# Kernel tuning notes

Measured on AMD Instinct MI355X. Metric: run time of the kernel, lower is better.

## Reference

```python
import jax, jax.numpy as jnp
import numpy as np

QMAX = 127.0          # int8 symmetric range
MMA_ALPHA = 1024.0    # leap mmaAlpha; applied to one scale and removed from the other (net no-op)
EPS = 1e-12


def _dynamic_quantize(t):
    """Per-tensor (blockSize=-1) symmetric int8 dynamic quantization."""
    s = jnp.maximum(jnp.max(jnp.abs(t)) / QMAX, EPS)
    q = jnp.clip(jnp.round(t / s), -QMAX, QMAX).astype(jnp.int8)
    return q, s


def setup_inputs() -> dict:
    key = jax.random.key(0)
    k1, k2 = jax.random.split(key)
    x = jax.random.normal(k1, (8192, 256), dtype=jnp.float32)   # [M, K]
    y = jax.random.normal(k2, (256, 8192), dtype=jnp.float32)   # [K, N]
    return {"x": x, "y": y}


def reference(x, y):
    x_q, x_s = _dynamic_quantize(x)
    y_q, y_s = _dynamic_quantize(y)
    # Integer accumulation (K=256 * 127^2 fits easily in int32), then dequantize.
    acc = jnp.matmul(x_q.astype(jnp.int32), y_q.astype(jnp.int32))  # [M, N] int32
    # mmaAlpha rescaling: scale one operand's scale up by alpha, the other down; cancels exactly.
    out = acc.astype(jnp.float32) * ((x_s * MMA_ALPHA) * (y_s / MMA_ALPHA))
    return out
```

## Files before the change

### kernel.cpp

```cpp
#include <hip/hip_runtime.h>

#define M_DIM 8192
#define N_DIM 8192
#define K_DIM 256

typedef __attribute__((ext_vector_type(4))) int i32x4;
typedef __attribute__((ext_vector_type(4))) float f32x4;

__device__ __forceinline__ void bar_lds() {
    asm volatile("s_waitcnt lgkmcnt(0)" ::: "memory");
    __builtin_amdgcn_sched_barrier(0);
    __builtin_amdgcn_s_barrier();
}

__device__ __forceinline__ void bar_stage() {
    asm volatile("s_waitcnt vmcnt(0) lgkmcnt(0)" ::: "memory");
    __builtin_amdgcn_sched_barrier(0);
    __builtin_amdgcn_s_barrier();
}

__device__ __forceinline__ void async_lds16(const signed char* g, signed char* l) {
    __builtin_amdgcn_global_load_lds(
        (const __attribute__((address_space(1))) void*)g,
        (__attribute__((address_space(3))) void*)l, 16, 0, 0);
}

__global__ __launch_bounds__(256) void absmax_kernel(const float* __restrict__ x,
                                                     const float* __restrict__ y,
                                                     float* __restrict__ partial) {
    const float* p = (blockIdx.y == 0) ? x : y;
    const int n4 = (M_DIM * K_DIM) / 4;
    const float4* p4 = (const float4*)p;
    float m = 0.0f;
    for (int i = blockIdx.x * 256 + threadIdx.x; i < n4; i += 256 * 256) {
        float4 v = p4[i];
        m = fmaxf(m, fmaxf(fmaxf(fabsf(v.x), fabsf(v.y)), fmaxf(fabsf(v.z), fabsf(v.w))));
    }
    for (int off = 32; off > 0; off >>= 1)
        m = fmaxf(m, __shfl_down(m, off));
    __shared__ float sm[4];
    int wid = threadIdx.x >> 6;
    if ((threadIdx.x & 63) == 0) sm[wid] = m;
    __syncthreads();
    if (threadIdx.x == 0)
        partial[blockIdx.y * 256 + blockIdx.x] = fmaxf(fmaxf(sm[0], sm[1]), fmaxf(sm[2], sm[3]));
}

__device__ __forceinline__ void load_scales(const float* __restrict__ partial,
                                            float& sx, float& sy, float* ssc) {
    const int tid = threadIdx.x;
    float mx = partial[tid];
    float my = partial[256 + tid];
    for (int off = 32; off > 0; off >>= 1) {
        mx = fmaxf(mx, __shfl_down(mx, off));
        my = fmaxf(my, __shfl_down(my, off));
    }
    if ((tid & 63) == 0) { ssc[tid >> 6] = mx; ssc[4 + (tid >> 6)] = my; }
    __syncthreads();
    mx = fmaxf(fmaxf(ssc[0], ssc[1]), fmaxf(ssc[2], ssc[3]));
    my = fmaxf(fmaxf(ssc[4], ssc[5]), fmaxf(ssc[6], ssc[7]));
    sx = fmaxf(mx / 127.0f, 1e-12f);
    sy = fmaxf(my / 127.0f, 1e-12f);
}

__device__ __forceinline__ int quant1(float v, float s) {
    float q = rintf(v / s);
    q = fmaxf(-127.0f, fminf(127.0f, q));
    return (int)q;
}

__global__ __launch_bounds__(256) void quant_kernel(const float* __restrict__ x,
                                                    const float* __restrict__ y,
                                                    unsigned int* __restrict__ xq_w,
                                                    signed char* __restrict__ yqt,
                                                    const float* __restrict__ partial) {
    __shared__ float ssc[8];
    __shared__ signed char tile[64][68];
    float sx, sy;
    load_scales(partial, sx, sy, ssc);
    int b = blockIdx.x;
    const int t = threadIdx.x;
    if (b < 2048) {
        int i = b * 256 + t;
        float4 v = ((const float4*)x)[i];
        unsigned b0 = (unsigned)quant1(v.x, sx) & 0xFF;
        unsigned b1 = (unsigned)quant1(v.y, sx) & 0xFF;
        unsigned b2 = (unsigned)quant1(v.z, sx) & 0xFF;
        unsigned b3 = (unsigned)quant1(v.w, sx) & 0xFF;
        xq_w[i] = b0 | (b1 << 8) | (b2 << 16) | (b3 << 24);
    } else {
        b -= 2048;
        const int n0 = (b & 127) * 64;
        const int k0 = (b >> 7) * 64;
        #pragma unroll
        for (int r = 0; r < 16; ++r) {
            int idx = r * 256 + t;
            int k = idx >> 6, n = idx & 63;
            float v = y[(size_t)(k0 + k) * N_DIM + n0 + n];
            tile[k][n] = (signed char)quant1(v, sy);
        }
        __syncthreads();
        #pragma unroll
        for (int r = 0; r < 4; ++r) {
            int idx = r * 256 + t;
            int n = idx >> 4, kw = idx & 15;
            unsigned w = ((unsigned)(unsigned char)tile[kw * 4 + 0][n])
                       | ((unsigned)(unsigned char)tile[kw * 4 + 1][n] << 8)
                       | ((unsigned)(unsigned char)tile[kw * 4 + 2][n] << 16)
                       | ((unsigned)(unsigned char)tile[kw * 4 + 3][n] << 24);
            *(unsigned*)(yqt + (size_t)(n0 + n) * K_DIM + k0 + kw * 4) = w;
        }
    }
}

__global__ __launch_bounds__(256) void gemm_i8_kernel(const signed char* __restrict__ xq,
                                                      const signed char* __restrict__ yqt,
                                                      const float* __restrict__ partial,
                                                      float* __restrict__ out) {
    __shared__ __align__(16) unsigned char smem[32 * 132 * 4];
    __shared__ float ssc[8];
    signed char* sA = (signed char*)smem;
    signed char* sB = sA + 128 * 64;
    float (*epi)[132] = (float(*)[132])smem;

    float sx, sy;
    load_scales(partial, sx, sy, ssc);
    const float scale = (sx * 1024.0f) * (sy / 1024.0f);

    const int tid = threadIdx.x;
    const int w = tid >> 6;
    const int lane = tid & 63;
    const int wr = w >> 1, wc = w & 1;

    const signed char* gbase = (w < 2)
        ? (xq  + (size_t)(blockIdx.y * 128 + (w & 1) * 64 + (lane >> 2)) * K_DIM + (lane & 3) * 16)
        : (yqt + (size_t)(blockIdx.x * 128 + (w & 1) * 64 + (lane >> 2)) * K_DIM + (lane & 3) * 16);
    signed char* lbase = ((w < 2) ? sA : sB) + (w & 1) * 64 * 64;

    const int frow = lane & 15;
    const int fk = (lane >> 4) * 16;
    const signed char* ard = sA + (wr * 64 + frow) * 64 + fk;
    const signed char* brd = sB + (wc * 64 + frow) * 64 + fk;

    i32x4 acc[4][4] = {};
    #pragma unroll
    for (int ks = 0; ks < 4; ++ks) {
        if (ks) bar_lds();
        #pragma unroll
        for (int c = 0; c < 4; ++c)
            async_lds16(gbase + (size_t)(c * 16) * K_DIM + ks * 64, lbase + c * 16 * 64);
        bar_stage();
        i32x4 a[4], b[4];
        #pragma unroll
        for (int mi = 0; mi < 4; ++mi)
            a[mi] = *(const i32x4*)(ard + mi * 16 * 64);
        #pragma unroll
        for (int ni = 0; ni < 4; ++ni)
            b[ni] = *(const i32x4*)(brd + ni * 16 * 64);
        #pragma unroll
        for (int mi = 0; mi < 4; ++mi)
            #pragma unroll
            for (int ni = 0; ni < 4; ++ni)
                acc[mi][ni] = __builtin_amdgcn_mfma_i32_16x16x64_i8(a[mi], b[ni], acc[mi][ni], 0, 0, 0);
    }
    bar_lds();

    const int qrow = (lane >> 4) * 4;
    const int qcol = lane & 15;
    #pragma unroll
    for (int mi = 0; mi < 4; ++mi) {
        if (mi) bar_lds();
        #pragma unroll
        for (int ni = 0; ni < 4; ++ni)
            #pragma unroll
            for (int r = 0; r < 4; ++r)
                epi[wr * 16 + qrow + r][wc * 64 + ni * 16 + qcol] =
                    (float)acc[mi][ni][r] * scale;
        bar_lds();
        #pragma unroll
        for (int i = 0; i < 4; ++i) {
            int row = i * 8 + (tid >> 5);
            int col4 = tid & 31;
            f32x4 v = *(const f32x4*)&epi[row][col4 * 4];
            int grow = blockIdx.y * 128 + (row >> 4) * 64 + mi * 16 + (row & 15);
            int gcol = blockIdx.x * 128 + col4 * 4;
            __builtin_nontemporal_store(v, (f32x4*)&out[(size_t)grow * N_DIM + gcol]);
        }
    }
}

extern "C" void kernel_launch(void* const* d_in, const int* in_sizes, int n_in,
                              void* d_out, int out_size, void* d_ws, size_t ws_size,
                              hipStream_t stream) {
    const float* x = (const float*)d_in[0];
    const float* y = (const float*)d_in[1];
    float* out = (float*)d_out;

    unsigned char* ws = (unsigned char*)d_ws;
    float* partial = (float*)ws;
    signed char* xq = (signed char*)(ws + 4096);
    signed char* yqt = xq + (size_t)M_DIM * K_DIM;

    absmax_kernel<<<dim3(256, 2), 256, 0, stream>>>(x, y, partial);

    quant_kernel<<<2048 + 512, 256, 0, stream>>>(x, y, (unsigned int*)xq, yqt, partial);

    gemm_i8_kernel<<<dim3(N_DIM / 128, M_DIM / 128), 256, 0, stream>>>(xq, yqt, partial, out);
}
```

Before: 68.63 us.

## Reshape GEMM block tile to 64x256 with each wave owning a 64-column strip

Changes the int8 GEMM block tile from 128x128 (2x2 waves) to 64 rows by 256 columns, with all four waves sharing the same A rows and each taking a 64-column slice of B. Loads and the epilogue staging buffer are rewritten to match, and the grid becomes 32x128. The intent is to make each output row segment wider for more contiguous stores and to change the A/B load balance. LDS use rises and B traffic per block grows, so the total global load volume shifts toward B.

```diff
diff --git a/kernel.cpp b/kernel.cpp
--- a/kernel.cpp
+++ b/kernel.cpp
@@ -117,11 +117,11 @@
                                                       const signed char* __restrict__ yqt,
                                                       const float* __restrict__ partial,
                                                       float* __restrict__ out) {
-    __shared__ __align__(16) unsigned char smem[32 * 132 * 4];
+    __shared__ __align__(16) unsigned char smem[20480];
     __shared__ float ssc[8];
     signed char* sA = (signed char*)smem;
-    signed char* sB = sA + 128 * 64;
-    float (*epi)[132] = (float(*)[132])smem;
+    signed char* sB = (signed char*)smem + 4096;
+    float (*epi)[260] = (float(*)[260])smem;
 
     float sx, sy;
     load_scales(partial, sx, sy, ssc);
@@ -130,26 +130,28 @@
     const int tid = threadIdx.x;
     const int w = tid >> 6;
     const int lane = tid & 63;
-    const int wr = w >> 1, wc = w & 1;
-
-    const signed char* gbase = (w < 2)
-        ? (xq  + (size_t)(blockIdx.y * 128 + (w & 1) * 64 + (lane >> 2)) * K_DIM + (lane & 3) * 16)
-        : (yqt + (size_t)(blockIdx.x * 128 + (w & 1) * 64 + (lane >> 2)) * K_DIM + (lane & 3) * 16);
-    signed char* lbase = ((w < 2) ? sA : sB) + (w & 1) * 64 * 64;
+    const int by = blockIdx.y;
+    const int bx = blockIdx.x;
 
     const int frow = lane & 15;
     const int fk = (lane >> 4) * 16;
-    const signed char* ard = sA + (wr * 64 + frow) * 64 + fk;
-    const signed char* brd = sB + (wc * 64 + frow) * 64 + fk;
+
+    const signed char* ag = xq + (size_t)(by * 64 + (tid >> 2)) * K_DIM + (tid & 3) * 16;
 
     i32x4 acc[4][4] = {};
     #pragma unroll
     for (int ks = 0; ks < 4; ++ks) {
         if (ks) bar_lds();
-        #pragma unroll
-        for (int c = 0; c < 4; ++c)
-            async_lds16(gbase + (size_t)(c * 16) * K_DIM + ks * 64, lbase + c * 16 * 64);
+        async_lds16(ag + ks * 64, sA + tid * 16);
+        #pragma unroll
+        for (int c = 0; c < 4; ++c) {
+            int i = c * 256 + tid;
+            async_lds16(yqt + (size_t)(bx * 256 + (i >> 2)) * K_DIM + (i & 3) * 16 + ks * 64,
+                        sB + i * 16);
+        }
         bar_stage();
+        const signed char* ard = sA + frow * 64 + fk;
+        const signed char* brd = sB + (w * 64 + frow) * 64 + fk;
         i32x4 a[4], b[4];
         #pragma unroll
         for (int mi = 0; mi < 4; ++mi)
@@ -174,16 +176,16 @@
         for (int ni = 0; ni < 4; ++ni)
             #pragma unroll
             for (int r = 0; r < 4; ++r)
-                epi[wr * 16 + qrow + r][wc * 64 + ni * 16 + qcol] =
-                    (float)acc[mi][ni][r] * scale;
+                epi[qrow + r][w * 64 + ni * 16 + qcol] = (float)acc[mi][ni][r] * scale;
         bar_lds();
         #pragma unroll
-        for (int i = 0; i < 4; ++i) {
-            int row = i * 8 + (tid >> 5);
-            int col4 = tid & 31;
-            f32x4 v = *(const f32x4*)&epi[row][col4 * 4];
-            int grow = blockIdx.y * 128 + (row >> 4) * 64 + mi * 16 + (row & 15);
-            int gcol = blockIdx.x * 128 + col4 * 4;
+        for (int j = 0; j < 4; ++j) {
+            int f4 = j * 256 + tid;
+            int row = f4 >> 6;
+            int c4 = f4 & 63;
+            f32x4 v = *(const f32x4*)&epi[row][c4 * 4];
+            int grow = by * 64 + mi * 16 + row;
+            int gcol = bx * 256 + c4 * 4;
             __builtin_nontemporal_store(v, (f32x4*)&out[(size_t)grow * N_DIM + gcol]);
         }
     }
@@ -205,5 +207,5 @@
 
     quant_kernel<<<2048 + 512, 256, 0, stream>>>(x, y, (unsigned int*)xq, yqt, partial);
 
-    gemm_i8_kernel<<<dim3(N_DIM / 128, M_DIM / 128), 256, 0, stream>>>(xq, yqt, partial, out);
-}
+    gemm_i8_kernel<<<dim3(N_DIM / 256, M_DIM / 64), 256, 0, stream>>>(xq, yqt, partial, out);
+}
```

After: 69.89 us. About the same (+1.8%).
